# Performance work log

Measured on AMD Instinct MI355X. Metric: run time of the kernel, lower is better.

Reference implementation:

```python
import jax, jax.numpy as jnp
import numpy as np

B, T, D, H, L, O = 256, 512, 64, 256, 2, 4


def _lstm_layer(x_tbd, W_ih, W_hh, b_ih, b_hh):
    """x_tbd: (T, B, D_in) -> hidden sequence (T, B, H). PyTorch gate order i,f,g,o."""
    Bb = x_tbd.shape[1]
    Hh = W_hh.shape[1]
    b = b_ih + b_hh
    # precompute input projections for all timesteps in one GEMM
    xW = jnp.einsum('tbd,gd->tbg', x_tbd, W_ih) + b  # (T, B, 4H)

    def step(carry, xw_t):
        h, c = carry
        gates = xw_t + h @ W_hh.T
        i, f, g, o = jnp.split(gates, 4, axis=-1)
        i = jax.nn.sigmoid(i)
        f = jax.nn.sigmoid(f)
        g = jnp.tanh(g)
        o = jax.nn.sigmoid(o)
        c = f * c + i * g
        h = o * jnp.tanh(c)
        return (h, c), h

    init = (jnp.zeros((Bb, Hh), x_tbd.dtype), jnp.zeros((Bb, Hh), x_tbd.dtype))
    _, hs = jax.lax.scan(step, init, xW)
    return hs


def setup_inputs() -> dict:
    key = jax.random.key(0)
    ks = jax.random.split(key, 11)
    s = 1.0 / np.sqrt(H)  # PyTorch LSTM init scale
    inp = {
        'x': jax.random.normal(ks[0], (B, T, D), dtype=jnp.float32),
        'W_ih0': jax.random.uniform(ks[1], (4 * H, D), minval=-s, maxval=s, dtype=jnp.float32),
        'W_hh0': jax.random.uniform(ks[2], (4 * H, H), minval=-s, maxval=s, dtype=jnp.float32),
        'b_ih0': jax.random.uniform(ks[3], (4 * H,), minval=-s, maxval=s, dtype=jnp.float32),
        'b_hh0': jax.random.uniform(ks[4], (4 * H,), minval=-s, maxval=s, dtype=jnp.float32),
        'W_ih1': jax.random.uniform(ks[5], (4 * H, H), minval=-s, maxval=s, dtype=jnp.float32),
        'W_hh1': jax.random.uniform(ks[6], (4 * H, H), minval=-s, maxval=s, dtype=jnp.float32),
        'b_ih1': jax.random.uniform(ks[7], (4 * H,), minval=-s, maxval=s, dtype=jnp.float32),
        'b_hh1': jax.random.uniform(ks[8], (4 * H,), minval=-s, maxval=s, dtype=jnp.float32),
        'fc_W': jax.random.uniform(ks[9], (O, H), minval=-s, maxval=s, dtype=jnp.float32),
        'fc_b': jax.random.uniform(ks[10], (O,), minval=-s, maxval=s, dtype=jnp.float32),
    }
    return inp


def reference(x, W_ih0, W_hh0, b_ih0, b_hh0, W_ih1, W_hh1, b_ih1, b_hh1, fc_W, fc_b):
    xt = jnp.transpose(x, (1, 0, 2))            # (T, B, D), batch_first -> time-major
    h1 = _lstm_layer(xt, W_ih0, W_hh0, b_ih0, b_hh0)   # (T, B, H)
    h2 = _lstm_layer(h1, W_ih1, W_hh1, b_ih1, b_hh1)   # (T, B, H)
    last = h2[-1]                                # out[:, -1, :] in batch_first layout
    return last @ fc_W.T + fc_b                  # (B, O)
```

## Files before the change

### kernel.cpp

```cpp
#include <hip/hip_runtime.h>


#define TT 512
#define HH 256
#define DD 64

typedef __attribute__((ext_vector_type(2))) _Float16 h2t;
typedef __attribute__((ext_vector_type(8))) _Float16 f16x8;
typedef __attribute__((ext_vector_type(4))) float f32x4;
typedef unsigned long long u64;
typedef unsigned u32;

__device__ __forceinline__ u32 pkh(float x, float y) {
    h2t h; h.x = (_Float16)x; h.y = (_Float16)y;
    return __builtin_bit_cast(u32, h);
}
__device__ __forceinline__ float sigf(float x) { return 1.f / (1.f + __expf(-x)); }
__device__ __forceinline__ float tanhf_(float x) {
    float e = __expf(2.f * x);
    return 1.f - 2.f / (e + 1.f);
}
__device__ __forceinline__ f16x8 ld8(const float* p) {
    float4 u = ((const float4*)p)[0];
    float4 v = ((const float4*)p)[1];
    f16x8 r = {(_Float16)u.x, (_Float16)u.y, (_Float16)u.z, (_Float16)u.w,
               (_Float16)v.x, (_Float16)v.y, (_Float16)v.z, (_Float16)v.w};
    return r;
}
__device__ __forceinline__ u32 ld32(const u32* p) {
    return __hip_atomic_load(p, __ATOMIC_RELAXED, __HIP_MEMORY_SCOPE_AGENT);
}
__device__ __forceinline__ void st32(u32* p, u32 v) {
    __hip_atomic_store(p, v, __ATOMIC_RELAXED, __HIP_MEMORY_SCOPE_AGENT);
}
__device__ __forceinline__ u64 ld64(const u64* p) {
    return __hip_atomic_load(p, __ATOMIC_RELAXED, __HIP_MEMORY_SCOPE_AGENT);
}
__device__ __forceinline__ void st64(u64* p, u64 v) {
    __hip_atomic_store(p, v, __ATOMIC_RELAXED, __HIP_MEMORY_SCOPE_AGENT);
}

__global__ __launch_bounds__(512, 2) void lstm_persist(
    const float* __restrict__ x,
    const float* __restrict__ Wih0, const float* __restrict__ Whh0,
    const float* __restrict__ bih0, const float* __restrict__ bhh0,
    const float* __restrict__ Wih1, const float* __restrict__ Whh1,
    const float* __restrict__ bih1, const float* __restrict__ bhh1,
    const float* __restrict__ fcW, const float* __restrict__ fcb,
    float* __restrict__ out,
    u64* h0ring, u64* h1ring, u32* cflagsA)
{
    __shared__ __align__(16) _Float16 sB[9216];
    __shared__ __align__(16) float part2[2][8][276];

    const int tid  = threadIdx.x;
    const int g    = blockIdx.x & 31;
    const int role = blockIdx.x >> 5;
    const bool isL1 = role >= 4;
    const int q = role & 3;
    const int batch0 = g * 8;
    u64* ring0 = h0ring + (size_t)g * 4096;
    u64* ring1 = h1ring + (size_t)g * 4096;
    u32* cflag = cflagsA + (size_t)g * 16;

    const int lane = tid & 63, w = tid >> 6;
    const int mw = w & 3, kh = w >> 2;
    const int bcol = lane & 15, kc = lane >> 4;

    const int n_ = tid & 127;
    const int jA = tid >> 7;
    const int jB = 4 + (tid >> 7);
    const int nq = n_ >> 5;

    const int R0 = mw * 256 + 64 * q + (lane & 15);
    const int R1 = R0 + 16, R2 = R0 + 32, R3 = R0 + 48;

#define DECL_TI(ti) f16x8 A##ti##_0={},A##ti##_1={},A##ti##_2={},A##ti##_3={}, \
                          A##ti##_4={},A##ti##_5={},A##ti##_6={},A##ti##_7={};
    DECL_TI(0) DECL_TI(1) DECL_TI(2) DECL_TI(3)
#undef DECL_TI

    if (isL1) {
#define LDA1(ti,j) { int k_ = (kh*8+(j))*32 + kc*8;                          \
        A##ti##_##j = ld8(k_ < 256 ? Wih1 + (size_t)R##ti*256 + k_           \
                                   : Whh1 + (size_t)R##ti*256 + (k_-256)); }
#define LDA1T(ti) LDA1(ti,0) LDA1(ti,1) LDA1(ti,2) LDA1(ti,3) \
                  LDA1(ti,4) LDA1(ti,5) LDA1(ti,6) LDA1(ti,7)
        LDA1T(0) LDA1T(1) LDA1T(2) LDA1T(3)
#undef LDA1T
#undef LDA1
    } else {
#define LDA0(ti,j) { int k_ = (kh*5+(j))*32 + kc*8;                          \
        A##ti##_##j = ld8(k_ < 64 ? Wih0 + (size_t)R##ti*64 + k_             \
                                  : Whh0 + (size_t)R##ti*256 + (k_-64)); }
#define LDA0T(ti) LDA0(ti,0) LDA0(ti,1) LDA0(ti,2) LDA0(ti,3) LDA0(ti,4)
        LDA0T(0) LDA0T(1) LDA0T(2) LDA0T(3)
#undef LDA0T
#undef LDA0
    }

    const float* bA = isL1 ? bih1 : bih0;
    const float* bB = isL1 ? bhh1 : bhh0;
    const float bz0 = bA[      64*q + lane] + bB[      64*q + lane];
    const float bz1 = bA[256 + 64*q + lane] + bB[256 + 64*q + lane];
    const float bz2 = bA[512 + 64*q + lane] + bB[512 + 64*q + lane];
    const float bz3 = bA[768 + 64*q + lane] + bB[768 + 64*q + lane];
    float cst = 0.f;

    u32* const sBu = (u32*)sB;
    for (int i = tid; i < 4608; i += 512) sBu[i] = 0;
    __syncthreads();

    if (!isL1 && tid >= 256 && tid < 384) {
        int t2 = tid - 256, j = t2 >> 4, c = t2 & 15;
        float4 v = ((const float4*)(x + ((size_t)(batch0 + j) * TT) * DD))[c];
        int bidx = (c >> 1) * 72 + j * 4 + (c & 1) * 2;
        sBu[bidx]     = pkh(v.x, v.y);
        sBu[bidx + 1] = pkh(v.z, v.w);
    }

    for (int s = 0; s <= TT; ++s) {
        __syncthreads();
        if (tid == 0) st32(&cflag[role], (u32)(s + 1));

        const bool act_ = isL1 ? (s >= 1) : (s < TT);
        const int  snx  = s + 1;
        const bool stg0 = (!isL1) && (snx < TT);
        const bool stg1 = isL1 && (snx <= TT);

        u32 cpre = 0xFFFFFFFFu;
        if (act_ && lane < 8) cpre = ld32(&cflag[lane]);

        u64 v0A = 0, v0B = 0, v1A = 0, v1B = 0;
        bool k0A = true, k0B = true, k1A = true, k1B = true;
        const u64 *p0A = nullptr, *p0B = nullptr, *p1A = nullptr, *p1B = nullptr;
        if (stg0 || stg1) {
            if (!(!isL1 && nq == q)) {
                const u64* b0 = ring0 + (size_t)((snx - 1) & 3) * 1024
                                + (nq << 8) + (n_ & 31);
                p0A = b0 + jA * 32; p0B = b0 + jB * 32;
                v0A = ld64(p0A); v0B = ld64(p0B);
                k0A = false; k0B = false;
            }
            if (stg1 && !(nq == q && snx >= 2)) {
                const u64* b1 = ring1 + (size_t)((snx + 2) & 3) * 1024
                                + (nq << 8) + (n_ & 31);
                p1A = b1 + jA * 32; p1B = b1 + jB * 32;
                v1A = ld64(p1A); v1B = ld64(p1B);
                k1A = false; k1B = false;
            }
        }
        float4 xreg;
        const bool doX = stg0 && (tid >= 256) && (tid < 384);
        if (doX) {
            int t2 = tid - 256, j = t2 >> 4, c = t2 & 15;
            xreg = ((const float4*)(x + ((size_t)(batch0 + j) * TT + snx) * DD))[c];
        }
        __builtin_amdgcn_sched_barrier(0);

        if (act_) {
            f32x4 C0 = {0,0,0,0}, C1 = {0,0,0,0}, C2 = {0,0,0,0}, C3 = {0,0,0,0};
#define MST(j, ktb) { const f16x8 Bf = *(const f16x8*)(sB + (((ktb)+(j))*4 + kc)*144 + bcol*8); \
            C0 = __builtin_amdgcn_mfma_f32_16x16x32_f16(A0_##j, Bf, C0, 0,0,0); \
            C1 = __builtin_amdgcn_mfma_f32_16x16x32_f16(A1_##j, Bf, C1, 0,0,0); \
            C2 = __builtin_amdgcn_mfma_f32_16x16x32_f16(A2_##j, Bf, C2, 0,0,0); \
            C3 = __builtin_amdgcn_mfma_f32_16x16x32_f16(A3_##j, Bf, C3, 0,0,0); }
            if (isL1) {
                const int ktb = kh * 8;
                MST(0,ktb) MST(1,ktb) MST(2,ktb) MST(3,ktb)
                MST(4,ktb) MST(5,ktb) MST(6,ktb) MST(7,ktb)
            } else {
                const int ktb = kh * 5;
                MST(0,ktb) MST(1,ktb) MST(2,ktb) MST(3,ktb) MST(4,ktb)
            }
#undef MST
            if (bcol < 8) {
                *(f32x4*)&part2[kh][bcol][mw*64 +  0 + kc*4] = C0;
                *(f32x4*)&part2[kh][bcol][mw*64 + 16 + kc*4] = C1;
                *(f32x4*)&part2[kh][bcol][mw*64 + 32 + kc*4] = C2;
                *(f32x4*)&part2[kh][bcol][mw*64 + 48 + kc*4] = C3;
            }
        }
        __syncthreads();

        if (act_) {
            float s0 = part2[0][w][      lane] + part2[1][w][      lane] + bz0;
            float s1 = part2[0][w][ 64 + lane] + part2[1][w][ 64 + lane] + bz1;
            float s2 = part2[0][w][128 + lane] + part2[1][w][128 + lane] + bz2;
            float s3 = part2[0][w][192 + lane] + part2[1][w][192 + lane] + bz3;
            float fi = sigf(s0), ff = sigf(s1), fg = tanhf_(s2), fo = sigf(s3);
            cst = ff * cst + fi * fg;
            float h = fo * tanhf_(cst);
            float hn = __shfl_down(h, 1);
            u32 hw = pkh(h, hn);

            if (!(lane & 1)) {
                int nn = (64 * q + lane) >> 1;
                int base = isL1 ? 32 : 8;
                sBu[(base + (nn >> 2)) * 72 + w * 4 + (nn & 3)] = hw;
            }

            const int tgt = s - 2;
            while (!__all(lane >= 8 || (int)cpre >= tgt)) {
                __builtin_amdgcn_s_sleep(1);
                if (lane < 8) cpre = ld32(&cflag[lane]);
            }
            if (!(lane & 1)) {
                u64 v = ((u64)(u32)(s + 1) << 32) | (u64)hw;
                u64* dst = (isL1 ? ring1 + (size_t)((s - 1) & 3) * 1024
                                 : ring0 + (size_t)(s & 3) * 1024)
                           + q * 256 + w * 32 + (lane >> 1);
                st64(dst, v);
            }
        }

        if (stg0 || stg1) {
            const u32 e0 = (u32)snx;
            const u32 e1 = (snx >= 2) ? (u32)snx : 0u;
            for (;;) {
                if (!k0A && (u32)(v0A >> 32) == e0) k0A = true;
                if (!k0B && (u32)(v0B >> 32) == e0) k0B = true;
                if (!k1A && (u32)(v1A >> 32) == e1) k1A = true;
                if (!k1B && (u32)(v1B >> 32) == e1) k1B = true;
                if (k0A & k0B & k1A & k1B) break;
                if (!k0A) v0A = ld64(p0A);
                if (!k0B) v0B = ld64(p0B);
                if (!k1A) v1A = ld64(p1A);
                if (!k1B) v1B = ld64(p1B);
            }
            if (p0A) {
                const int base = isL1 ? 0 : 8;
                sBu[(base + (n_ >> 2)) * 72 + jA * 4 + (n_ & 3)] = (u32)v0A;
                sBu[(base + (n_ >> 2)) * 72 + jB * 4 + (n_ & 3)] = (u32)v0B;
            }
            if (p1A) {
                sBu[(32 + (n_ >> 2)) * 72 + jA * 4 + (n_ & 3)] = (u32)v1A;
                sBu[(32 + (n_ >> 2)) * 72 + jB * 4 + (n_ & 3)] = (u32)v1B;
            }
            if (doX) {
                int t2 = tid - 256, j = t2 >> 4, c = t2 & 15;
                int bidx = (c >> 1) * 72 + j * 4 + (c & 1) * 2;
                sBu[bidx]     = pkh(xreg.x, xreg.y);
                sBu[bidx + 1] = pkh(xreg.z, xreg.w);
            }
        }
    }

    if (isL1 && q == 0) {
        const u32 ef = (u32)(TT + 1);
#pragma unroll
        for (int pp = 0; pp < 2; ++pp) {
            int p = tid + pp * 512;
            int j = p >> 7, n = p & 127;
            const u64* a = ring1 + 3 * 1024 + (n >> 5) * 256 + j * 32 + (n & 31);
            u64 v;
            do { v = ld64(a); } while ((u32)(v >> 32) != ef);
            sBu[j * 128 + n] = (u32)v;
        }
        __syncthreads();
        const int j = tid >> 6, l2 = tid & 63;
        const int o = l2 >> 4, kk = l2 & 15;
        float ssum = 0.f;
#pragma unroll
        for (int m = 0; m < 16; ++m) {
            int k = kk * 16 + m;
            ssum += (float)sB[j * 256 + k] * fcW[o * HH + k];
        }
#pragma unroll
        for (int off = 8; off; off >>= 1) ssum += __shfl_down(ssum, off);
        if (kk == 0) out[(batch0 + j) * 4 + o] = ssum + fcb[o];
    }
}

extern "C" void kernel_launch(void* const* d_in, const int* in_sizes, int n_in,
                              void* d_out, int out_size, void* d_ws, size_t ws_size,
                              hipStream_t stream)
{
    (void)in_sizes; (void)n_in; (void)out_size; (void)ws_size;
    const float* x    = (const float*)d_in[0];
    const float* Wih0 = (const float*)d_in[1];
    const float* Whh0 = (const float*)d_in[2];
    const float* bih0 = (const float*)d_in[3];
    const float* bhh0 = (const float*)d_in[4];
    const float* Wih1 = (const float*)d_in[5];
    const float* Whh1 = (const float*)d_in[6];
    const float* bih1 = (const float*)d_in[7];
    const float* bhh1 = (const float*)d_in[8];
    const float* fcW  = (const float*)d_in[9];
    const float* fcb  = (const float*)d_in[10];
    float* out = (float*)d_out;

    u64* h0ring = (u64*)d_ws;
    u64* h1ring = (u64*)((char*)d_ws + 1048576);
    u32* cflags = (u32*)((char*)d_ws + 2097152);

    hipMemsetAsync(d_ws, 0, 2097152 + 2048, stream);

    lstm_persist<<<dim3(256), dim3(512), 0, stream>>>(
        x, Wih0, Whh0, bih0, bhh0, Wih1, Whh1, bih1, bhh1, fcW, fcb, out,
        h0ring, h1ring, cflags);
}
```

Baseline: 1.428 ms.

## Defer ring-buffer hidden-state prefetch until after gate compute and drop local LDS write

Moves the initial polling loads of the neighbour hidden-state ring buffers from before the MFMA step to after the gate nonlinearity, and removes the sched_barrier. Each block now reads its own slice back from the global ring instead of writing its new h directly into shared memory. The final epilogue read is restructured into a dual-address polling loop. This trades early prefetch overlap for a simpler flow, at the cost of extra global round trips for the block's own data and possibly longer waits on the critical recurrent path.

```diff
diff --git a/kernel.cpp b/kernel.cpp
--- a/kernel.cpp
+++ b/kernel.cpp
@@ -66,11 +66,6 @@
     const int lane = tid & 63, w = tid >> 6;
     const int mw = w & 3, kh = w >> 2;
     const int bcol = lane & 15, kc = lane >> 4;
-
-    const int n_ = tid & 127;
-    const int jA = tid >> 7;
-    const int jB = 4 + (tid >> 7);
-    const int nq = n_ >> 5;
 
     const int R0 = mw * 256 + 64 * q + (lane & 15);
     const int R1 = R0 + 16, R2 = R0 + 32, R3 = R0 + 48;
@@ -114,7 +109,7 @@
     if (!isL1 && tid >= 256 && tid < 384) {
         int t2 = tid - 256, j = t2 >> 4, c = t2 & 15;
         float4 v = ((const float4*)(x + ((size_t)(batch0 + j) * TT) * DD))[c];
-        int bidx = (c >> 1) * 72 + j * 4 + (c & 1) * 2;
+        int bidx = (c >> 1) * 72 + j * 4 + 2 * (c & 1);
         sBu[bidx]     = pkh(v.x, v.y);
         sBu[bidx + 1] = pkh(v.z, v.w);
     }
@@ -128,35 +123,14 @@
         const bool stg0 = (!isL1) && (snx < TT);
         const bool stg1 = isL1 && (snx <= TT);
 
-        u32 cpre = 0xFFFFFFFFu;
+        u32 cpre = 0u;
         if (act_ && lane < 8) cpre = ld32(&cflag[lane]);
-
-        u64 v0A = 0, v0B = 0, v1A = 0, v1B = 0;
-        bool k0A = true, k0B = true, k1A = true, k1B = true;
-        const u64 *p0A = nullptr, *p0B = nullptr, *p1A = nullptr, *p1B = nullptr;
-        if (stg0 || stg1) {
-            if (!(!isL1 && nq == q)) {
-                const u64* b0 = ring0 + (size_t)((snx - 1) & 3) * 1024
-                                + (nq << 8) + (n_ & 31);
-                p0A = b0 + jA * 32; p0B = b0 + jB * 32;
-                v0A = ld64(p0A); v0B = ld64(p0B);
-                k0A = false; k0B = false;
-            }
-            if (stg1 && !(nq == q && snx >= 2)) {
-                const u64* b1 = ring1 + (size_t)((snx + 2) & 3) * 1024
-                                + (nq << 8) + (n_ & 31);
-                p1A = b1 + jA * 32; p1B = b1 + jB * 32;
-                v1A = ld64(p1A); v1B = ld64(p1B);
-                k1A = false; k1B = false;
-            }
-        }
-        float4 xreg;
+        float4 xr;
         const bool doX = stg0 && (tid >= 256) && (tid < 384);
         if (doX) {
             int t2 = tid - 256, j = t2 >> 4, c = t2 & 15;
-            xreg = ((const float4*)(x + ((size_t)(batch0 + j) * TT + snx) * DD))[c];
-        }
-        __builtin_amdgcn_sched_barrier(0);
+            xr = ((const float4*)(x + ((size_t)(batch0 + j) * TT + snx) * DD))[c];
+        }
 
         if (act_) {
             f32x4 C0 = {0,0,0,0}, C1 = {0,0,0,0}, C2 = {0,0,0,0}, C3 = {0,0,0,0};
@@ -194,12 +168,6 @@
             float hn = __shfl_down(h, 1);
             u32 hw = pkh(h, hn);
 
-            if (!(lane & 1)) {
-                int nn = (64 * q + lane) >> 1;
-                int base = isL1 ? 32 : 8;
-                sBu[(base + (nn >> 2)) * 72 + w * 4 + (nn & 3)] = hw;
-            }
-
             const int tgt = s - 2;
             while (!__all(lane >= 8 || (int)cpre >= tgt)) {
                 __builtin_amdgcn_s_sleep(1);
@@ -215,48 +183,70 @@
         }
 
         if (stg0 || stg1) {
+            const int n0  = tid & 127;
+            const int jj0 = tid >> 7, jj1 = 4 + jj0;
+            const u64* b0 = ring0 + (size_t)((snx - 1) & 3) * 1024
+                            + ((n0 >> 5) << 8) + (n0 & 31);
+            const u64* a00 = b0 + jj0 * 32;
+            const u64* a01 = b0 + jj1 * 32;
+            u64 v00, v01, v10 = 0, v11 = 0;
+            const u64 *a10 = nullptr, *a11 = nullptr;
+            if (isL1) {
+                const u64* b1 = ring1 + (size_t)((snx + 2) & 3) * 1024
+                                + ((n0 >> 5) << 8) + (n0 & 31);
+                a10 = b1 + jj0 * 32; a11 = b1 + jj1 * 32;
+                v00 = ld64(a00); v01 = ld64(a01);
+                v10 = ld64(a10); v11 = ld64(a11);
+            } else {
+                v00 = ld64(a00); v01 = ld64(a01);
+            }
             const u32 e0 = (u32)snx;
             const u32 e1 = (snx >= 2) ? (u32)snx : 0u;
             for (;;) {
-                if (!k0A && (u32)(v0A >> 32) == e0) k0A = true;
-                if (!k0B && (u32)(v0B >> 32) == e0) k0B = true;
-                if (!k1A && (u32)(v1A >> 32) == e1) k1A = true;
-                if (!k1B && (u32)(v1B >> 32) == e1) k1B = true;
-                if (k0A & k0B & k1A & k1B) break;
-                if (!k0A) v0A = ld64(p0A);
-                if (!k0B) v0B = ld64(p0B);
-                if (!k1A) v1A = ld64(p1A);
-                if (!k1B) v1B = ld64(p1B);
-            }
-            if (p0A) {
-                const int base = isL1 ? 0 : 8;
-                sBu[(base + (n_ >> 2)) * 72 + jA * 4 + (n_ & 3)] = (u32)v0A;
-                sBu[(base + (n_ >> 2)) * 72 + jB * 4 + (n_ & 3)] = (u32)v0B;
-            }
-            if (p1A) {
-                sBu[(32 + (n_ >> 2)) * 72 + jA * 4 + (n_ & 3)] = (u32)v1A;
-                sBu[(32 + (n_ >> 2)) * 72 + jB * 4 + (n_ & 3)] = (u32)v1B;
+                bool k0 = ((u32)(v00 >> 32) == e0);
+                bool k1 = ((u32)(v01 >> 32) == e0);
+                bool k2 = !isL1 || ((u32)(v10 >> 32) == e1);
+                bool k3 = !isL1 || ((u32)(v11 >> 32) == e1);
+                if (k0 & k1 & k2 & k3) break;
+                if (!k0) v00 = ld64(a00);
+                if (!k1) v01 = ld64(a01);
+                if (isL1) {
+                    if (!k2) v10 = ld64(a10);
+                    if (!k3) v11 = ld64(a11);
+                }
+            }
+            const int cb0 = isL1 ? 0 : 8;
+            sBu[(cb0 + (n0 >> 2)) * 72 + jj0 * 4 + (n0 & 3)] = (u32)v00;
+            sBu[(cb0 + (n0 >> 2)) * 72 + jj1 * 4 + (n0 & 3)] = (u32)v01;
+            if (isL1) {
+                sBu[(32 + (n0 >> 2)) * 72 + jj0 * 4 + (n0 & 3)] = (u32)v10;
+                sBu[(32 + (n0 >> 2)) * 72 + jj1 * 4 + (n0 & 3)] = (u32)v11;
             }
             if (doX) {
                 int t2 = tid - 256, j = t2 >> 4, c = t2 & 15;
-                int bidx = (c >> 1) * 72 + j * 4 + (c & 1) * 2;
-                sBu[bidx]     = pkh(xreg.x, xreg.y);
-                sBu[bidx + 1] = pkh(xreg.z, xreg.w);
+                int bidx = (c >> 1) * 72 + j * 4 + 2 * (c & 1);
+                sBu[bidx]     = pkh(xr.x, xr.y);
+                sBu[bidx + 1] = pkh(xr.z, xr.w);
             }
         }
     }
 
     if (isL1 && q == 0) {
         const u32 ef = (u32)(TT + 1);
-#pragma unroll
-        for (int pp = 0; pp < 2; ++pp) {
-            int p = tid + pp * 512;
-            int j = p >> 7, n = p & 127;
-            const u64* a = ring1 + 3 * 1024 + (n >> 5) * 256 + j * 32 + (n & 31);
-            u64 v;
-            do { v = ld64(a); } while ((u32)(v >> 32) != ef);
-            sBu[j * 128 + n] = (u32)v;
-        }
+        const int n0  = tid & 127;
+        const int jj0 = tid >> 7, jj1 = 4 + jj0;
+        const u64* b = ring1 + 3 * 1024 + ((n0 >> 5) << 8) + (n0 & 31);
+        const u64* a0 = b + jj0 * 32;
+        const u64* a1 = b + jj1 * 32;
+        u64 v0 = ld64(a0), v1 = ld64(a1);
+        for (;;) {
+            bool k0 = ((u32)(v0 >> 32) == ef), k1 = ((u32)(v1 >> 32) == ef);
+            if (k0 & k1) break;
+            if (!k0) v0 = ld64(a0);
+            if (!k1) v1 = ld64(a1);
+        }
+        sBu[jj0 * 128 + n0] = (u32)v0;
+        sBu[jj1 * 128 + n0] = (u32)v1;
         __syncthreads();
         const int j = tid >> 6, l2 = tid & 63;
         const int o = l2 >> 4, kk = l2 & 15;
```

Measured after the change: 1.319 ms. 7.7% less time.
